# Kernel optimization log

Hardware: AMD Instinct MI355X
Metric: run time of the kernel (lower is better)

## Reference

```python
import jax, jax.numpy as jnp
import numpy as np

MARGIN = 0.1  # init kwarg: margin
# type_of_distance='euclidean', type_of_quadruplets='hard', what_is_hard='one'


def _distance_euclidean(x):
    # l2-normalize rows, then all-pairs euclidean distance (torch.cdist p=2)
    x = x / jnp.linalg.norm(x, axis=1, keepdims=True)
    sq = jnp.sum(x * x, axis=1)
    d2 = sq[:, None] + sq[None, :] - 2.0 * (x @ x.T)
    return jnp.sqrt(jnp.maximum(d2, 0.0))


def setup_inputs() -> dict:
    key = jax.random.key(0)
    k1, k2 = jax.random.split(key)
    B, D, C = 256, 512, 80
    logits = jax.random.normal(k1, (B, D), dtype=jnp.float32)
    # sparse multi-hot labels: ~2.4 active classes per sample
    labels = (jax.random.uniform(k2, (B, C)) < 0.03).astype(jnp.float32)
    return {"logits": logits, "labels": labels}


def reference(logits, labels):
    n = labels.shape[0]
    sames = (labels @ labels.T) > 0                      # [B,B] bool
    diffs = ~sames
    sames = sames & ~jnp.eye(n, dtype=bool)              # fill_diagonal_(0)
    triu = jnp.triu(jnp.ones((n, n), dtype=bool), k=1)   # J < K
    # O(B^3) quadruplet-candidate mask: sames[I,J] & sames[I,K] & (J<K)
    mask = sames[:, :, None] & sames[:, None, :] & triu[None, :, :]
    I, J, K = jnp.nonzero(mask)                          # row-major, same as torch.where
    # expand each (I,J,K) triplet with every negative N of anchor I
    rows, cols = jnp.nonzero(diffs[I])                   # [n_quads]
    quadruplets = jnp.stack([I[rows], J[rows], K[rows], cols], axis=1)

    mat = _distance_euclidean(jax.lax.stop_gradient(logits))  # logits.detach()
    Ii, Jj, Kk, Nn = quadruplets[:, 0], quadruplets[:, 1], quadruplets[:, 2], quadruplets[:, 3]
    ij = mat[Ii, Jj]
    ik = mat[Ii, Kk]
    innd = mat[Ii, Nn]
    m1 = innd - ij
    m2 = innd - ik
    # type_of_quadruplets='hard', what_is_hard='one' (opt = OR)
    cond = ((m1 <= MARGIN) | (m2 <= MARGIN)) & ((m1 <= 0) | (m2 <= 0))
    return quadruplets[cond]
```

## Files before the change

### kernel.cpp

```cpp
#include <hip/hip_runtime.h>
#include <math.h>

#define NB 256
#define ND 512
#define NC 80
#define NSPLIT 8
#define SLOT 32640

__device__ float g_x [NB * ND];
__device__ float g_xt[ND * NB];
__device__ float g_sq[NB];
__device__ float g_ddneg[NB * NB];
__device__ unsigned long long g_m[NB * 2];
__device__ int   g_atot[NB];
__device__ int   g_T[NB];
__device__ int4  g_trip[NB * SLOT];

__device__ __forceinline__ int block_scan(int val, int* tmp) {
    int tid = threadIdx.x;
    __syncthreads();
    tmp[tid] = val;
    __syncthreads();
    #pragma unroll
    for (int off = 1; off < 256; off <<= 1) {
        int v = (tid >= off) ? tmp[tid - off] : 0;
        __syncthreads();
        tmp[tid] += v;
        __syncthreads();
    }
    return tmp[tid];
}

__device__ __forceinline__ int ubcount(const float* s, float thr) {
    int pos = 0;
    #pragma unroll
    for (int step = 128; step > 0; step >>= 1) {
        int np = pos + step;
        if (s[np - 1] <= thr) pos = np;
    }
    return pos;
}

__global__ __launch_bounds__(256) void k_prep(const float* __restrict__ logits,
                                              const float* __restrict__ labels) {
    int b = blockIdx.x, tid = threadIdx.x;
    __shared__ double red[NB];
    float v0 = logits[b * ND + tid];
    float v1 = logits[b * ND + 256 + tid];
    red[tid] = (double)(v0 * v0) + (double)(v1 * v1);
    __syncthreads();
    for (int off = 128; off > 0; off >>= 1) {
        if (tid < off) red[tid] += red[tid + off];
        __syncthreads();
    }
    float S = (float)red[0];
    float nrm = sqrtf(S);
    __syncthreads();
    float a0 = v0 / nrm;
    float a1 = v1 / nrm;
    g_x[b * ND + tid]          = a0;
    g_x[b * ND + 256 + tid]    = a1;
    g_xt[tid * NB + b]         = a0;
    g_xt[(tid + 256) * NB + b] = a1;
    red[tid] = (double)(a0 * a0) + (double)(a1 * a1);
    __syncthreads();
    for (int off = 128; off > 0; off >>= 1) {
        if (tid < off) red[tid] += red[tid + off];
        __syncthreads();
    }
    if (tid == 0) g_sq[b] = (float)red[0];
    int wv = tid >> 6, ln = tid & 63;
    if (wv == 0) {
        unsigned long long m0 = __ballot(labels[b * NC + ln] != 0.0f);
        if (ln == 0) g_m[2 * b] = m0;
    } else if (wv == 1) {
        bool p = (ln < 16) ? (labels[b * NC + 64 + ln] != 0.0f) : false;
        unsigned long long m1 = __ballot(p);
        if (ln == 0) g_m[2 * b + 1] = m1;
    }
}

__global__ __launch_bounds__(256) void k_count() {
    __shared__ float xi[ND];
    __shared__ float s_dd[NB], s_ddneg[NB], s_sort[NB];
    __shared__ int s_tmp[NB], s_rowbase[NB];
    __shared__ short s_plist[NB];
    int i = blockIdx.x, tid = threadIdx.x;
    xi[tid]       = g_x[i * ND + tid];
    xi[tid + 256] = g_x[i * ND + 256 + tid];
    __syncthreads();
    double dot = 0.0;
    #pragma unroll 8
    for (int c = 0; c < ND; ++c)
        dot = fma((double)xi[c], (double)g_xt[c * NB + tid], dot);
    float dotf = (float)dot;
    float sm   = g_sq[i] + g_sq[tid];
    float d2   = sm - 2.0f * dotf;
    float dv   = sqrtf(d2 > 0.0f ? d2 : 0.0f);
    s_dd[tid] = dv;
    unsigned long long mi0 = g_m[2 * i],   mi1 = g_m[2 * i + 1];
    unsigned long long mt0 = g_m[2 * tid], mt1 = g_m[2 * tid + 1];
    bool shl   = ((mi0 & mt0) | (mi1 & mt1)) != 0ULL;
    bool isPos = shl && (tid != i);
    float ddneg = shl ? INFINITY : dv;
    s_ddneg[tid] = ddneg;
    g_ddneg[i * NB + tid] = ddneg;
    int incl = block_scan(isPos ? 1 : 0, s_tmp);
    int P = s_tmp[255];
    if (isPos) s_plist[incl - 1] = (short)tid;
    if (tid < P - 1) s_rowbase[tid] = tid * (P - 1) - (tid * (tid - 1)) / 2;
    float v = ddneg;
    for (int k = 2; k <= 256; k <<= 1)
        for (int j = k >> 1; j > 0; j >>= 1) {
            float oth;
            if (j >= 64) {
                __syncthreads();
                s_sort[tid] = v;
                __syncthreads();
                oth = s_sort[tid ^ j];
            } else {
                oth = __shfl_xor(v, j);
            }
            bool keepmin = (((tid & k) == 0) == ((tid & j) == 0));
            v = keepmin ? fminf(v, oth) : fmaxf(v, oth);
        }
    __syncthreads();
    s_sort[tid] = v;
    __syncthreads();
    int T = P * (P - 1) / 2;
    if (tid == 0) g_T[i] = T;
    int carried = 0;
    for (int cb = 0; cb < T; cb += NB) {
        int t = cb + tid;
        int cnt = 0, jk = 0;
        float thr = 0.0f;
        if (t < T) {
            int a = 0;
            #pragma unroll
            for (int step = 128; step > 0; step >>= 1) {
                int na = a + step;
                if (na <= P - 2 && s_rowbase[na] <= t) a = na;
            }
            int b = a + 1 + (t - s_rowbase[a]);
            int jj = s_plist[a], kk = s_plist[b];
            thr = fmaxf(s_dd[jj], s_dd[kk]);
            jk  = jj | (kk << 8);
            cnt = ubcount(s_sort, thr);
        }
        int inc2 = block_scan(cnt, s_tmp);
        if (t < T)
            g_trip[i * SLOT + t] =
                make_int4(jk, __float_as_int(thr), carried + inc2 - cnt, 0);
        carried += s_tmp[255];
    }
    if (tid == 0) g_atot[i] = carried;
}

__global__ __launch_bounds__(256) void k_write(int4* __restrict__ out, int maxQuads) {
    int i = blockIdx.x / NSPLIT;
    int split = blockIdx.x % NSPLIT;
    int tid = threadIdx.x;
    int wv = tid >> 6, ln = tid & 63;
    int psum = 0;
    for (int m = ln; m < i; m += 64) psum += g_atot[m];
    #pragma unroll
    for (int off = 1; off < 64; off <<= 1) psum += __shfl_xor(psum, off);
    int anchorBase = psum;
    float vneg[4];
    #pragma unroll
    for (int r = 0; r < 4; ++r) vneg[r] = g_ddneg[i * NB + ((r << 6) | ln)];
    unsigned long long lanemask = (1ULL << ln) - 1ULL;
    int T = g_T[i];
    int waveId = (split << 2) | wv;
    int t = waveId;
    int4 tr = (t < T) ? g_trip[i * SLOT + t] : make_int4(0, 0, 0, 0);
    while (t < T) {
        int tn = t + NSPLIT * 4;
        int4 nxt = (tn < T) ? g_trip[i * SLOT + tn] : make_int4(0, 0, 0, 0);
        int jj = tr.x & 255, kk = tr.x >> 8;
        float thr = __int_as_float(tr.y);
        int base = anchorBase + tr.z;
        bool f0 = (vneg[0] <= thr), f1 = (vneg[1] <= thr);
        bool f2 = (vneg[2] <= thr), f3 = (vneg[3] <= thr);
        unsigned long long m0 = __ballot(f0), m1 = __ballot(f1);
        unsigned long long m2 = __ballot(f2), m3 = __ballot(f3);
        int b1 = base + __popcll(m0);
        int b2 = b1 + __popcll(m1);
        int b3 = b2 + __popcll(m2);
        if (f0) { int pos = base + __popcll(m0 & lanemask);
                  if (pos < maxQuads) out[pos] = make_int4(i, jj, kk, ln); }
        if (f1) { int pos = b1 + __popcll(m1 & lanemask);
                  if (pos < maxQuads) out[pos] = make_int4(i, jj, kk, 64 | ln); }
        if (f2) { int pos = b2 + __popcll(m2 & lanemask);
                  if (pos < maxQuads) out[pos] = make_int4(i, jj, kk, 128 | ln); }
        if (f3) { int pos = b3 + __popcll(m3 & lanemask);
                  if (pos < maxQuads) out[pos] = make_int4(i, jj, kk, 192 | ln); }
        tr = nxt;
        t = tn;
    }
}

extern "C" void kernel_launch(void* const* d_in, const int* in_sizes, int n_in,
                              void* d_out, int out_size, void* d_ws, size_t ws_size,
                              hipStream_t stream) {
    const float* logits = (const float*)d_in[0];
    const float* labels = (const float*)d_in[1];
    if (n_in >= 2 && in_sizes[0] == NB * NC && in_sizes[1] == NB * ND) {
        logits = (const float*)d_in[1];
        labels = (const float*)d_in[0];
    }
    int maxQuads = out_size / 4;

    k_prep <<<NB, NB, 0, stream>>>(logits, labels);
    k_count<<<NB, NB, 0, stream>>>();
    k_write<<<NB * NSPLIT, NB, 0, stream>>>((int4*)d_out, maxQuads);
}
```

Measured before the change: 191.7 us.

## Flatten triplet work across anchors with global cursor and shuffle-based scans

Triplets from all anchors are packed into one compact global array using an atomic cursor, and each triplet now carries its anchor id. The write kernel then strides uniformly over the flat list instead of giving each anchor a fixed set of waves, which evens out load across anchors with very different triplet counts. A separate single-block kernel computes per-anchor output bases, and the shared-memory Hillis-Steele block scan is replaced with a wave-shuffle scan. In exchange, each triplet iteration reloads the anchor's negative-distance row and output base from global memory instead of keeping them in registers.

```diff
diff --git a/kernel.cpp b/kernel.cpp
--- a/kernel.cpp
+++ b/kernel.cpp
@@ -6,6 +6,7 @@
 #define NC 80
 #define NSPLIT 8
 #define SLOT 32640
+#define KW_WAVES (NB * NSPLIT * 4)
 
 __device__ float g_x [NB * ND];
 __device__ float g_xt[ND * NB];
@@ -13,22 +14,25 @@
 __device__ float g_ddneg[NB * NB];
 __device__ unsigned long long g_m[NB * 2];
 __device__ int   g_atot[NB];
-__device__ int   g_T[NB];
+__device__ int   g_abase[NB];
+__device__ int   g_cursor;
 __device__ int4  g_trip[NB * SLOT];
 
-__device__ __forceinline__ int block_scan(int val, int* tmp) {
-    int tid = threadIdx.x;
-    __syncthreads();
-    tmp[tid] = val;
-    __syncthreads();
+__device__ __forceinline__ int block_scan_int(int val, int* wsum) {
+    int tid = threadIdx.x, wv = tid >> 6, ln = tid & 63;
+    int v = val;
     #pragma unroll
-    for (int off = 1; off < 256; off <<= 1) {
-        int v = (tid >= off) ? tmp[tid - off] : 0;
-        __syncthreads();
-        tmp[tid] += v;
-        __syncthreads();
-    }
-    return tmp[tid];
+    for (int off = 1; off < 64; off <<= 1) {
+        int u = __shfl_up(v, off);
+        v += (ln >= off) ? u : 0;
+    }
+    __syncthreads();
+    if (ln == 63) wsum[wv] = v;
+    __syncthreads();
+    int add = 0;
+    #pragma unroll
+    for (int w = 0; w < 4; ++w) if (w < wv) add += wsum[w];
+    return v + add;
 }
 
 __device__ __forceinline__ int ubcount(const float* s, float thr) {
@@ -45,6 +49,7 @@
                                               const float* __restrict__ labels) {
     int b = blockIdx.x, tid = threadIdx.x;
     __shared__ double red[NB];
+    if (b == 0 && tid == 0) g_cursor = 0;
     float v0 = logits[b * ND + tid];
     float v1 = logits[b * ND + 256 + tid];
     red[tid] = (double)(v0 * v0) + (double)(v1 * v1);
@@ -82,8 +87,8 @@
 
 __global__ __launch_bounds__(256) void k_count() {
     __shared__ float xi[ND];
-    __shared__ float s_dd[NB], s_ddneg[NB], s_sort[NB];
-    __shared__ int s_tmp[NB], s_rowbase[NB];
+    __shared__ float s_dd[NB], s_sort[NB];
+    __shared__ int s_w4[4], s_rowbase[NB], s_base;
     __shared__ short s_plist[NB];
     int i = blockIdx.x, tid = threadIdx.x;
     xi[tid]       = g_x[i * ND + tid];
@@ -103,10 +108,9 @@
     bool shl   = ((mi0 & mt0) | (mi1 & mt1)) != 0ULL;
     bool isPos = shl && (tid != i);
     float ddneg = shl ? INFINITY : dv;
-    s_ddneg[tid] = ddneg;
     g_ddneg[i * NB + tid] = ddneg;
-    int incl = block_scan(isPos ? 1 : 0, s_tmp);
-    int P = s_tmp[255];
+    int incl = block_scan_int(isPos ? 1 : 0, s_w4);
+    int P = s_w4[0] + s_w4[1] + s_w4[2] + s_w4[3];
     if (isPos) s_plist[incl - 1] = (short)tid;
     if (tid < P - 1) s_rowbase[tid] = tid * (P - 1) - (tid * (tid - 1)) / 2;
     float v = ddneg;
@@ -126,9 +130,10 @@
         }
     __syncthreads();
     s_sort[tid] = v;
-    __syncthreads();
     int T = P * (P - 1) / 2;
-    if (tid == 0) g_T[i] = T;
+    if (tid == 0) s_base = (T > 0) ? atomicAdd(&g_cursor, T) : 0;
+    __syncthreads();
+    int dbase = s_base;
     int carried = 0;
     for (int cb = 0; cb < T; cb += NB) {
         int t = cb + tid;
@@ -147,54 +152,57 @@
             jk  = jj | (kk << 8);
             cnt = ubcount(s_sort, thr);
         }
-        int inc2 = block_scan(cnt, s_tmp);
+        int inc2 = block_scan_int(cnt, s_w4);
+        int chunkTot = s_w4[0] + s_w4[1] + s_w4[2] + s_w4[3];
         if (t < T)
-            g_trip[i * SLOT + t] =
-                make_int4(jk, __float_as_int(thr), carried + inc2 - cnt, 0);
-        carried += s_tmp[255];
+            g_trip[dbase + t] =
+                make_int4(jk, __float_as_int(thr), carried + inc2 - cnt, i);
+        carried += chunkTot;
     }
     if (tid == 0) g_atot[i] = carried;
 }
 
+__global__ __launch_bounds__(256) void k_abase() {
+    __shared__ int s_w4[4];
+    int tid = threadIdx.x;
+    int v = g_atot[tid];
+    int incl = block_scan_int(v, s_w4);
+    g_abase[tid] = incl - v;
+}
+
 __global__ __launch_bounds__(256) void k_write(int4* __restrict__ out, int maxQuads) {
-    int i = blockIdx.x / NSPLIT;
-    int split = blockIdx.x % NSPLIT;
     int tid = threadIdx.x;
     int wv = tid >> 6, ln = tid & 63;
-    int psum = 0;
-    for (int m = ln; m < i; m += 64) psum += g_atot[m];
-    #pragma unroll
-    for (int off = 1; off < 64; off <<= 1) psum += __shfl_xor(psum, off);
-    int anchorBase = psum;
-    float vneg[4];
-    #pragma unroll
-    for (int r = 0; r < 4; ++r) vneg[r] = g_ddneg[i * NB + ((r << 6) | ln)];
+    int W = (blockIdx.x << 2) | wv;
+    int Ttot = g_cursor;
     unsigned long long lanemask = (1ULL << ln) - 1ULL;
-    int T = g_T[i];
-    int waveId = (split << 2) | wv;
-    int t = waveId;
-    int4 tr = (t < T) ? g_trip[i * SLOT + t] : make_int4(0, 0, 0, 0);
-    while (t < T) {
-        int tn = t + NSPLIT * 4;
-        int4 nxt = (tn < T) ? g_trip[i * SLOT + tn] : make_int4(0, 0, 0, 0);
+    int t = W;
+    int4 tr = (t < Ttot) ? g_trip[t] : make_int4(0, 0, 0, 0);
+    while (t < Ttot) {
+        int tn = t + KW_WAVES;
+        int4 nxt = (tn < Ttot) ? g_trip[tn] : make_int4(0, 0, 0, 0);
+        int ai = tr.w;
+        const float* row = g_ddneg + ai * NB;
+        float v0 = row[ln], v1 = row[64 + ln];
+        float v2 = row[128 + ln], v3 = row[192 + ln];
+        int base = g_abase[ai] + tr.z;
         int jj = tr.x & 255, kk = tr.x >> 8;
         float thr = __int_as_float(tr.y);
-        int base = anchorBase + tr.z;
-        bool f0 = (vneg[0] <= thr), f1 = (vneg[1] <= thr);
-        bool f2 = (vneg[2] <= thr), f3 = (vneg[3] <= thr);
+        bool f0 = (v0 <= thr), f1 = (v1 <= thr);
+        bool f2 = (v2 <= thr), f3 = (v3 <= thr);
         unsigned long long m0 = __ballot(f0), m1 = __ballot(f1);
         unsigned long long m2 = __ballot(f2), m3 = __ballot(f3);
         int b1 = base + __popcll(m0);
         int b2 = b1 + __popcll(m1);
         int b3 = b2 + __popcll(m2);
         if (f0) { int pos = base + __popcll(m0 & lanemask);
-                  if (pos < maxQuads) out[pos] = make_int4(i, jj, kk, ln); }
+                  if (pos < maxQuads) out[pos] = make_int4(ai, jj, kk, ln); }
         if (f1) { int pos = b1 + __popcll(m1 & lanemask);
-                  if (pos < maxQuads) out[pos] = make_int4(i, jj, kk, 64 | ln); }
+                  if (pos < maxQuads) out[pos] = make_int4(ai, jj, kk, 64 | ln); }
         if (f2) { int pos = b2 + __popcll(m2 & lanemask);
-                  if (pos < maxQuads) out[pos] = make_int4(i, jj, kk, 128 | ln); }
+                  if (pos < maxQuads) out[pos] = make_int4(ai, jj, kk, 128 | ln); }
         if (f3) { int pos = b3 + __popcll(m3 & lanemask);
-                  if (pos < maxQuads) out[pos] = make_int4(i, jj, kk, 192 | ln); }
+                  if (pos < maxQuads) out[pos] = make_int4(ai, jj, kk, 192 | ln); }
         tr = nxt;
         t = tn;
     }
@@ -213,5 +221,6 @@
 
     k_prep <<<NB, NB, 0, stream>>>(logits, labels);
     k_count<<<NB, NB, 0, stream>>>();
+    k_abase<<<1,  NB, 0, stream>>>();
     k_write<<<NB * NSPLIT, NB, 0, stream>>>((int4*)d_out, maxQuads);
 }
```

Result: faster. 187.6 us (-2.2%).
